# Kernel optimization log

Hardware: AMD Instinct MI355X
Metric: run time of the kernel (lower is better)

The kernel has to match this reference:

```python
import jax, jax.numpy as jnp
import numpy as np

N = 100000   # nodes
E = 1600000  # edges
B = 256      # graphs in batch
IN_DIM = 128
OUT_DIM = 64


def setup_inputs() -> dict:
    key = jax.random.key(0)
    ks = jax.random.split(key, 8)
    x = jax.random.normal(ks[0], (N, IN_DIM), dtype=jnp.float32)
    edge_index = jax.random.randint(ks[1], (2, E), 0, N)
    edge_weight = jax.random.uniform(ks[2], (E,), dtype=jnp.float32)
    batch = jnp.sort(jax.random.randint(ks[3], (N,), 0, B))
    # learned params (GCNConv: x @ W + b with glorot-ish scale)
    W1 = jax.random.normal(ks[4], (IN_DIM, OUT_DIM), dtype=jnp.float32) * 0.05
    b1 = jnp.zeros((OUT_DIM,), dtype=jnp.float32)
    W2 = jax.random.normal(ks[5], (OUT_DIM, OUT_DIM), dtype=jnp.float32) * 0.05
    b2 = jnp.zeros((OUT_DIM,), dtype=jnp.float32)
    return {"x": x, "edge_index": edge_index, "edge_weight": edge_weight,
            "batch": batch, "W1": W1, "b1": b1, "W2": W2, "b2": b2}


def _gcn_conv(x, W, b, src, dst, w, n):
    # PyG GCNConv (normalize=True, add_self_loops already applied by caller):
    # out[dst] += D^-1/2[src] * w * D^-1/2[dst] * (x @ W)[src]
    xw = x @ W
    deg = jax.ops.segment_sum(w, dst, num_segments=n)
    dinv = jnp.where(deg > 0, jax.lax.rsqrt(deg), 0.0)
    norm = dinv[src] * w * dinv[dst]
    out = jax.ops.segment_sum(norm[:, None] * xw[src], dst, num_segments=n)
    return out + b


def reference(x, edge_index, edge_weight, batch, W1, b1, W2, b2):
    n = x.shape[0]
    loop = jnp.arange(n)
    # add self loops with weight 1 (GCNConv default fill_value=1.0)
    src = jnp.concatenate([edge_index[0], loop])
    dst = jnp.concatenate([edge_index[1], loop])
    w = jnp.concatenate([edge_weight, jnp.ones((n,), x.dtype)])

    h = _gcn_conv(x, W1, b1, src, dst, w, n)
    h = _gcn_conv(h, W2, b2, src, dst, w, n)

    # deterministic pairwise clustering (stand-in for randomized graclus matching)
    n_clusters = n // 2
    cluster = loop // 2
    # max_pool_x: per-cluster feature max, cluster batch id = min over members
    xp = jax.ops.segment_max(h, cluster, num_segments=n_clusters)
    bp = jax.ops.segment_min(batch, cluster, num_segments=n_clusters)
    # original loop: x[ind[0]:ind[1]].mean(0) over contiguous batch indices is a
    # single row => output per graph = first pooled node of that graph
    first = jax.ops.segment_min(jnp.arange(n_clusters), bp, num_segments=B)
    return xp[first]
```

## Files before the change

### kernel.cpp

```cpp
#include <hip/hip_runtime.h>
#include <climits>


#define NF_CAP 40960
#define CHUNK 8192
#define STRIDE 128
#define BK_BITS 8
#define NBMAX 512
#define MAXW 3200

__global__ void k_init(unsigned int* mark1w, unsigned char* mark2,
                       int* first, int* cnt, int* gcur, float* WW, float* bW,
                       const float* __restrict__ W1, const float* __restrict__ W2,
                       const float* __restrict__ b1, int n, int nb) {
  int i = blockIdx.x * blockDim.x + threadIdx.x;
  if (i < n) mark2[i] = 0;
  if (i < MAXW) mark1w[i] = 0;
  if (i < nb) first[i] = INT_MAX;
  if (i < 4) cnt[i] = 0;
  if (i < NBMAX) gcur[i] = 0;
  int t = threadIdx.x;
  int lane = t & 63, wv = t >> 6;
  if (blockIdx.x < 2) {
    int k0 = blockIdx.x * 64 + wv * 16;
#pragma unroll 1
    for (int k = k0; k < k0 + 16; ++k) {
      float acc = 0.f;
#pragma unroll 8
      for (int m = 0; m < 64; ++m)
        acc += W1[k * 64 + m] * W2[m * 64 + lane];
      WW[k * 64 + lane] = acc;
    }
  } else if (blockIdx.x == 2 && wv == 0) {
    float acc = 0.f;
#pragma unroll 8
    for (int m = 0; m < 64; ++m)
      acc += b1[m] * W2[m * 64 + lane];
    bW[lane] = acc;
  }
}

__global__ void k_firstsel(const int* __restrict__ batch, int* first,
                           unsigned int* mark1w, unsigned char* mark2,
                           int nc, int n) {
  int c = blockIdx.x * blockDim.x + threadIdx.x;
  if (c == 0) {
    mark2[n - 2] = 1; mark2[n - 1] = 1;
    atomicOr(&mark1w[(n - 2) >> 5], 1u << ((n - 2) & 31));
    atomicOr(&mark1w[(n - 1) >> 5], 1u << ((n - 1) & 31));
  }
  if (c >= nc) return;
  int b = batch[2 * c];
  if (c == 0 || batch[2 * c - 2] != b) {
    first[b] = c;
    int n0 = 2 * c;
    mark2[n0] = 1; mark2[n0 + 1] = 1;
    atomicOr(&mark1w[n0 >> 5], 3u << (n0 & 31));
  }
}

__global__ __launch_bounds__(1024) void k_bkt(const int* __restrict__ src,
    const int* __restrict__ dst, const float* __restrict__ w,
    const unsigned int* __restrict__ mark1w, unsigned char* mark2,
    int* gcur, uint2* bktbuf, int cap, int e) {
  __shared__ int scnt[NBMAX], sgb[NBMAX];
  int t = threadIdx.x;
  if (t < NBMAX) scnt[t] = 0;
  __syncthreads();
  int i0 = blockIdx.x * CHUNK;
  int rd[8], rs[8];
  float rw[8];
#pragma unroll
  for (int k = 0; k < 8; ++k) {
    int i = i0 + t + k * 1024;
    if (i < e) {
      int d = dst[i];
      int s = src[i];
      rd[k] = d; rs[k] = s; rw[k] = w[i];
      atomicAdd(&scnt[d >> BK_BITS], 1);
      if ((mark1w[d >> 5] >> (d & 31)) & 1u) mark2[s] = 1;
    } else {
      rd[k] = -1;
    }
  }
  __syncthreads();
  if (t < NBMAX) {
    int c = scnt[t];
    sgb[t] = c ? atomicAdd(&gcur[t], c) : 0;
    scnt[t] = 0;
  }
  __syncthreads();
#pragma unroll
  for (int k = 0; k < 8; ++k) {
    if (rd[k] >= 0) {
      int b = rd[k] >> BK_BITS;
      int pos = sgb[b] + atomicAdd(&scnt[b], 1);
      if (pos < cap)
        bktbuf[(size_t)b * cap + pos] =
            make_uint2(((unsigned int)rs[k] << BK_BITS) | (unsigned int)(rd[k] & 255),
                       __float_as_uint(rw[k]));
    }
  }
}

__global__ __launch_bounds__(256) void k_degscat(const int* __restrict__ gcur,
    const uint2* __restrict__ bktbuf, int cap, const unsigned char* __restrict__ mark2,
    int* cntF, int* fidx, int* list,
    float* dinv, int* counts2, int* fcols, float* fvals, int n) {
  __shared__ float acc[256];
  __shared__ int sfidx[256];
  __shared__ int lcur[256];
  __shared__ int sd[256];
  __shared__ int base_s;
  int t = threadIdx.x, b = blockIdx.x;
  int gbase = b << BK_BITS;
  int i = gbase + t;
  acc[t] = 0.f;
  int flag = (i < n && mark2[i]) ? 1 : 0;
  sd[t] = flag;
  __syncthreads();
  for (int off = 1; off < 256; off <<= 1) {
    int a = (t >= off) ? sd[t - off] : 0;
    __syncthreads();
    sd[t] += a;
    __syncthreads();
  }
  int incl = sd[t];
  if (t == 255) base_s = atomicAdd(cntF, incl);
  __syncthreads();
  int f0 = -1;
  if (flag) {
    int g = base_s + incl - 1;
    if (g < NF_CAP) { f0 = g; fidx[i] = g; list[g] = i; }
  }
  sfidx[t] = f0;
  lcur[t] = (f0 >= 0) ? f0 * STRIDE : 0;
  __syncthreads();
  int m = min(gcur[b], cap);
  const uint2* base = bktbuf + (size_t)b * cap;
  for (int j = t; j < m; j += 256) {
    uint2 u = base[j];
    int dl = (int)(u.x & 255u);
    float wv = __uint_as_float(u.y);
    atomicAdd(&acc[dl], wv);
    int f = sfidx[dl];
    if (f >= 0) {
      int pos = atomicAdd(&lcur[dl], 1);
      if (pos < (f + 1) * STRIDE) {
        fcols[pos] = (int)(u.x >> BK_BITS);
        fvals[pos] = wv;
      }
    }
  }
  __syncthreads();
  if (i < n) {
    dinv[i] = rsqrtf(1.0f + acc[t]);
    int f = sfidx[t];
    if (f >= 0) counts2[f] = min(lcur[t] - f * STRIDE, STRIDE);
  }
}

__global__ __launch_bounds__(256) void k_agg(const float* __restrict__ x,
    const int* __restrict__ list, const int* __restrict__ cntF,
    const int* __restrict__ counts2, const int* __restrict__ fcols,
    const float* __restrict__ fvals, const float* __restrict__ dinv,
    float* __restrict__ aggx) {
  int lane = threadIdx.x & 63;
  int half = lane >> 5, sub = lane & 31;
  int wid = (blockIdx.x * blockDim.x + threadIdx.x) >> 6;
  int nw = (gridDim.x * blockDim.x) >> 6;
  int m = min(*cntF, NF_CAP);
  const float4* x4 = (const float4*)x;
  float4* a4 = (float4*)aggx;
  for (int li = wid; li < m; li += nw) {
    int i = list[li];
    float dv = dinv[i];
    float4 xi = x4[(size_t)i * 32 + sub];
    float ax = 0.f, ay = 0.f, az = 0.f, aw = 0.f;
    int p = li * STRIDE;
    int end = p + counts2[li];
    while (p + 16 <= end) {
      int c[8]; float v[8]; float4 g[8];
#pragma unroll
      for (int j = 0; j < 8; ++j) {
        c[j] = fcols[p + 2 * j + half];
        v[j] = fvals[p + 2 * j + half];
      }
#pragma unroll
      for (int j = 0; j < 8; ++j) g[j] = x4[(size_t)c[j] * 32 + sub];
#pragma unroll
      for (int j = 0; j < 8; ++j) v[j] *= dinv[c[j]];
#pragma unroll
      for (int j = 0; j < 8; ++j) {
        ax += v[j] * g[j].x; ay += v[j] * g[j].y;
        az += v[j] * g[j].z; aw += v[j] * g[j].w;
      }
      p += 16;
    }
    while (p + 4 <= end) {
      int c0 = fcols[p + half], c1 = fcols[p + 2 + half];
      float v0 = fvals[p + half], v1 = fvals[p + 2 + half];
      float4 g0 = x4[(size_t)c0 * 32 + sub];
      float4 g1 = x4[(size_t)c1 * 32 + sub];
      v0 *= dinv[c0]; v1 *= dinv[c1];
      ax += v0 * g0.x + v1 * g1.x; ay += v0 * g0.y + v1 * g1.y;
      az += v0 * g0.z + v1 * g1.z; aw += v0 * g0.w + v1 * g1.w;
      p += 4;
    }
    while (p + 2 <= end) {
      int c = fcols[p + half];
      float v = fvals[p + half] * dinv[c];
      float4 g = x4[(size_t)c * 32 + sub];
      ax += v * g.x; ay += v * g.y; az += v * g.z; aw += v * g.w;
      p += 2;
    }
    if (p < end && half == 0) {
      int c = fcols[p];
      float v = fvals[p] * dinv[c];
      float4 g = x4[(size_t)c * 32 + sub];
      ax += v * g.x; ay += v * g.y; az += v * g.z; aw += v * g.w;
    }
    ax += __shfl(ax, lane ^ 32);
    ay += __shfl(ay, lane ^ 32);
    az += __shfl(az, lane ^ 32);
    aw += __shfl(aw, lane ^ 32);
    if (half == 0) {
      float4 r;
      r.x = dv * (ax + dv * xi.x);
      r.y = dv * (ay + dv * xi.y);
      r.z = dv * (az + dv * xi.z);
      r.w = dv * (aw + dv * xi.w);
      a4[(size_t)li * 32 + sub] = r;
    }
  }
}

__global__ __launch_bounds__(128) void k_h2out(const float* __restrict__ aggx,
    const int* __restrict__ first, const int* __restrict__ fidx,
    const int* __restrict__ counts2, const int* __restrict__ fcols,
    const float* __restrict__ fvals, const float* __restrict__ dinv,
    const float* __restrict__ WW, const float* __restrict__ bW,
    const float* __restrict__ b2, float* __restrict__ out, int nb, int nc) {
  __shared__ float Wl[128 * 64];
  __shared__ float sag[2][128];
  __shared__ float hh[2][64];
  int t = threadIdx.x;
  for (int p = t; p < 128 * 16; p += 128)
    ((float4*)Wl)[p] = ((const float4*)WW)[p];
  __syncthreads();
  int lane = t & 63, wv = t >> 6;
  int half = lane >> 5, sub = lane & 31;
  int b = blockIdx.x;
  if (b >= nb) return;
  int fc = min(first[b], nc - 1);
  int node = 2 * fc + wv;
  int f = fidx[node];
  float dv = dinv[node];
  const float4* a4 = (const float4*)aggx;
  float ax = 0.f, ay = 0.f, az = 0.f, aw = 0.f, sv = 0.f;
  int p = f * STRIDE;
  int end = p + counts2[f];
  while (p + 8 <= end) {
    int c[4]; float v[4]; int g[4]; float4 r[4];
#pragma unroll
    for (int j = 0; j < 4; ++j) {
      c[j] = fcols[p + 2 * j + half];
      v[j] = fvals[p + 2 * j + half];
    }
#pragma unroll
    for (int j = 0; j < 4; ++j) g[j] = fidx[c[j]];
#pragma unroll
    for (int j = 0; j < 4; ++j) v[j] *= dinv[c[j]];
#pragma unroll
    for (int j = 0; j < 4; ++j) r[j] = a4[(size_t)g[j] * 32 + sub];
#pragma unroll
    for (int j = 0; j < 4; ++j) {
      ax += v[j] * r[j].x; ay += v[j] * r[j].y;
      az += v[j] * r[j].z; aw += v[j] * r[j].w;
      sv += v[j];
    }
    p += 8;
  }
  while (p + 2 <= end) {
    int c = fcols[p + half];
    float v = fvals[p + half] * dinv[c];
    int g = fidx[c];
    float4 r = a4[(size_t)g * 32 + sub];
    ax += v * r.x; ay += v * r.y; az += v * r.z; aw += v * r.w;
    sv += v;
    p += 2;
  }
  if (p < end && half == 0) {
    int c = fcols[p];
    float v = fvals[p] * dinv[c];
    int g = fidx[c];
    float4 r = a4[(size_t)g * 32 + sub];
    ax += v * r.x; ay += v * r.y; az += v * r.z; aw += v * r.w;
    sv += v;
  }
  ax += __shfl(ax, lane ^ 32);
  ay += __shfl(ay, lane ^ 32);
  az += __shfl(az, lane ^ 32);
  aw += __shfl(aw, lane ^ 32);
  sv += __shfl(sv, lane ^ 32);
  float4 rs = a4[(size_t)f * 32 + sub];
  if (half == 0) {
    sag[wv][4 * sub + 0] = dv * (ax + dv * rs.x);
    sag[wv][4 * sub + 1] = dv * (ay + dv * rs.y);
    sag[wv][4 * sub + 2] = dv * (az + dv * rs.z);
    sag[wv][4 * sub + 3] = dv * (aw + dv * rs.w);
  }
  float sfin = dv * (sv + dv);
  __syncthreads();
  float o = b2[lane] + sfin * bW[lane];
#pragma unroll 8
  for (int k = 0; k < 128; ++k)
    o += sag[wv][k] * Wl[k * 64 + lane];
  hh[wv][lane] = o;
  __syncthreads();
  if (wv == 0)
    out[(size_t)b * 64 + lane] = fmaxf(hh[0][lane], hh[1][lane]);
}

extern "C" void kernel_launch(void* const* d_in, const int* in_sizes, int n_in,
                              void* d_out, int out_size, void* d_ws, size_t ws_size,
                              hipStream_t stream) {
  const float* x     = (const float*)d_in[0];
  const int*   ei    = (const int*)d_in[1];
  const float* ew    = (const float*)d_in[2];
  const int*   batch = (const int*)d_in[3];
  const float* W1    = (const float*)d_in[4];
  const float* b1    = (const float*)d_in[5];
  const float* W2    = (const float*)d_in[6];
  const float* b2    = (const float*)d_in[7];

  const int E  = in_sizes[2];
  const int N  = in_sizes[3];
  const int B  = out_size / 64;
  const int NC = N / 2;
  const int* srcI = ei;
  const int* dstI = ei + E;

  const int NBKT = (N + 255) >> BK_BITS;
  const int CAP  = ((E + NBKT - 1) / NBKT) * 2;

  char* p = (char*)d_ws;
  auto alloc = [&](size_t bytes) -> char* {
    char* r = p;
    p += (bytes + 255) & ~size_t(255);
    return r;
  };
  float* dinv    = (float*)alloc((size_t)N * 4);
  unsigned int* mark1w = (unsigned int*)alloc((size_t)MAXW * 4);
  unsigned char* mark2 = (unsigned char*)alloc(N);
  int*   fidx    = (int*)alloc((size_t)N * 4);
  int*   list    = (int*)alloc((size_t)NF_CAP * 4);
  int*   counts2 = (int*)alloc((size_t)NF_CAP * 4);
  int*   first   = (int*)alloc((size_t)B * 4);
  int*   cnt     = (int*)alloc(256);
  int*   gcur    = (int*)alloc(NBMAX * 4);
  float* WW      = (float*)alloc(128 * 64 * 4);
  float* bW      = (float*)alloc(64 * 4);
  uint2* bktbuf  = (uint2*)alloc((size_t)NBKT * CAP * 8);
  int*   fcols   = (int*)alloc((size_t)NF_CAP * STRIDE * 4);
  float* fvals   = (float*)alloc((size_t)NF_CAP * STRIDE * 4);
  float* aggx    = (float*)alloc((size_t)NF_CAP * 128 * 4);

  int gN = (N + 255) / 256;
  int gB = (E + CHUNK - 1) / CHUNK;
  int* cntF = cnt;

  k_init<<<gN, 256, 0, stream>>>(mark1w, mark2, first, cnt, gcur, WW, bW,
                                 W1, W2, b1, N, B);
  k_firstsel<<<(NC + 255) / 256, 256, 0, stream>>>(batch, first, mark1w, mark2, NC, N);
  k_bkt<<<gB, 1024, 0, stream>>>(srcI, dstI, ew, mark1w, mark2, gcur, bktbuf, CAP, E);
  k_degscat<<<NBKT, 256, 0, stream>>>(gcur, bktbuf, CAP, mark2, cntF, fidx, list,
                                      dinv, counts2, fcols, fvals, N);
  k_agg<<<2048, 256, 0, stream>>>(x, list, cntF, counts2, fcols, fvals, dinv, aggx);
  k_h2out<<<B, 128, 0, stream>>>(aggx, first, fidx, counts2, fcols, fvals, dinv,
                                 WW, bW, b2, (float*)d_out, B, NC);
}
```

Before: 99.50 us.

## Replace global-atomic bucket cursors with per-block slab slots and prefix scan

Edge bucketing no longer reserves space in each destination bucket with global atomicAdd on a shared cursor. Each source block now writes into its own fixed 64-entry slot per bucket and records a per-block count. The degree/scatter kernel prefix-scans those counts and finds each entry's slot by binary search. This removes global atomic contention and lets k_init clear mark2 with int-wide stores, at the cost of a scan, a binary search per element, and silently dropping edges when a block holds more than 64 for one bucket.

New measurement: 107.4 us. 7.9% more time.

```diff
diff --git a/kernel.cpp b/kernel.cpp
--- a/kernel.cpp
+++ b/kernel.cpp
@@ -8,17 +8,17 @@
 #define BK_BITS 8
 #define NBMAX 512
 #define MAXW 3200
-
-__global__ void k_init(unsigned int* mark1w, unsigned char* mark2,
-                       int* first, int* cnt, int* gcur, float* WW, float* bW,
+#define SLOT 64
+
+__global__ void k_init(unsigned int* mark1w, int* mark2i,
+                       int* first, int* cnt, float* WW, float* bW,
                        const float* __restrict__ W1, const float* __restrict__ W2,
-                       const float* __restrict__ b1, int n, int nb) {
+                       const float* __restrict__ b1, int n4, int nb) {
   int i = blockIdx.x * blockDim.x + threadIdx.x;
-  if (i < n) mark2[i] = 0;
+  if (i < n4) mark2i[i] = 0;
   if (i < MAXW) mark1w[i] = 0;
   if (i < nb) first[i] = INT_MAX;
   if (i < 4) cnt[i] = 0;
-  if (i < NBMAX) gcur[i] = 0;
   int t = threadIdx.x;
   int lane = t & 63, wv = t >> 6;
   if (blockIdx.x < 2) {
@@ -62,12 +62,13 @@
 __global__ __launch_bounds__(1024) void k_bkt(const int* __restrict__ src,
     const int* __restrict__ dst, const float* __restrict__ w,
     const unsigned int* __restrict__ mark1w, unsigned char* mark2,
-    int* gcur, uint2* bktbuf, int cap, int e) {
-  __shared__ int scnt[NBMAX], sgb[NBMAX];
+    int* cnt, uint2* slab, int e, int nbkt, int nblk) {
+  __shared__ int scnt[NBMAX];
   int t = threadIdx.x;
   if (t < NBMAX) scnt[t] = 0;
   __syncthreads();
-  int i0 = blockIdx.x * CHUNK;
+  int g = blockIdx.x;
+  int i0 = g * CHUNK;
   int rd[8], rs[8];
   float rw[8];
 #pragma unroll
@@ -84,9 +85,8 @@
     }
   }
   __syncthreads();
-  if (t < NBMAX) {
-    int c = scnt[t];
-    sgb[t] = c ? atomicAdd(&gcur[t], c) : 0;
+  if (t < nbkt) {
+    cnt[g * nbkt + t] = min(scnt[t], SLOT);
     scnt[t] = 0;
   }
   __syncthreads();
@@ -94,23 +94,25 @@
   for (int k = 0; k < 8; ++k) {
     if (rd[k] >= 0) {
       int b = rd[k] >> BK_BITS;
-      int pos = sgb[b] + atomicAdd(&scnt[b], 1);
-      if (pos < cap)
-        bktbuf[(size_t)b * cap + pos] =
+      int pos = atomicAdd(&scnt[b], 1);
+      if (pos < SLOT)
+        slab[((size_t)b * nblk + g) * SLOT + pos] =
             make_uint2(((unsigned int)rs[k] << BK_BITS) | (unsigned int)(rd[k] & 255),
                        __float_as_uint(rw[k]));
     }
   }
 }
 
-__global__ __launch_bounds__(256) void k_degscat(const int* __restrict__ gcur,
-    const uint2* __restrict__ bktbuf, int cap, const unsigned char* __restrict__ mark2,
+__global__ __launch_bounds__(256) void k_degscat(const int* __restrict__ cnt,
+    const uint2* __restrict__ slab, int nblk, int nbkt,
+    const unsigned char* __restrict__ mark2,
     int* cntF, int* fidx, int* list,
     float* dinv, int* counts2, int* fcols, float* fvals, int n) {
   __shared__ float acc[256];
   __shared__ int sfidx[256];
   __shared__ int lcur[256];
   __shared__ int sd[256];
+  __shared__ int pref[257];
   __shared__ int base_s;
   int t = threadIdx.x, b = blockIdx.x;
   int gbase = b << BK_BITS;
@@ -130,25 +132,44 @@
   __syncthreads();
   int f0 = -1;
   if (flag) {
-    int g = base_s + incl - 1;
-    if (g < NF_CAP) { f0 = g; fidx[i] = g; list[g] = i; }
+    int gidx = base_s + incl - 1;
+    if (gidx < NF_CAP) { f0 = gidx; fidx[i] = gidx; list[gidx] = i; }
   }
   sfidx[t] = f0;
   lcur[t] = (f0 >= 0) ? f0 * STRIDE : 0;
-  __syncthreads();
-  int m = min(gcur[b], cap);
-  const uint2* base = bktbuf + (size_t)b * cap;
-  for (int j = t; j < m; j += 256) {
-    uint2 u = base[j];
-    int dl = (int)(u.x & 255u);
-    float wv = __uint_as_float(u.y);
-    atomicAdd(&acc[dl], wv);
-    int f = sfidx[dl];
-    if (f >= 0) {
-      int pos = atomicAdd(&lcur[dl], 1);
-      if (pos < (f + 1) * STRIDE) {
-        fcols[pos] = (int)(u.x >> BK_BITS);
-        fvals[pos] = wv;
+  int v = (t < nblk) ? cnt[t * nbkt + b] : 0;
+  sd[t] = v;
+  __syncthreads();
+  for (int off = 1; off < 256; off <<= 1) {
+    int a = (t >= off) ? sd[t - off] : 0;
+    __syncthreads();
+    sd[t] += a;
+    __syncthreads();
+  }
+  pref[t + 1] = sd[t];
+  if (t == 0) pref[0] = 0;
+  __syncthreads();
+  int m = pref[nblk];
+  const uint2* sb = slab + (size_t)b * nblk * SLOT;
+  for (int j0 = 0; j0 < m; j0 += 256) {
+    int j = j0 + t;
+    if (j < m) {
+      int lo = 0, hi = nblk;
+      while (hi - lo > 1) {
+        int mid = (lo + hi) >> 1;
+        if (pref[mid] <= j) lo = mid; else hi = mid;
+      }
+      uint2 u = sb[(size_t)lo * SLOT + (j - pref[lo])];
+      int dl = (int)(u.x & 255u);
+      float wv = __uint_as_float(u.y);
+      atomicAdd(&acc[dl], wv);
+      int f = sfidx[dl];
+      if (f >= 0) {
+        int pos = atomicAdd(&lcur[dl], 1);
+        if (pos < (f + 1) * STRIDE) {
+          fcols[pos] = (int)(u.x >> BK_BITS);
+          fvals[pos] = wv;
+        }
       }
     }
   }
@@ -342,7 +363,7 @@
   const int* dstI = ei + E;
 
   const int NBKT = (N + 255) >> BK_BITS;
-  const int CAP  = ((E + NBKT - 1) / NBKT) * 2;
+  const int NBLK = (E + CHUNK - 1) / CHUNK;
 
   char* p = (char*)d_ws;
   auto alloc = [&](size_t bytes) -> char* {
@@ -352,30 +373,31 @@
   };
   float* dinv    = (float*)alloc((size_t)N * 4);
   unsigned int* mark1w = (unsigned int*)alloc((size_t)MAXW * 4);
-  unsigned char* mark2 = (unsigned char*)alloc(N);
+  unsigned char* mark2 = (unsigned char*)alloc((size_t)(N + 4));
   int*   fidx    = (int*)alloc((size_t)N * 4);
   int*   list    = (int*)alloc((size_t)NF_CAP * 4);
   int*   counts2 = (int*)alloc((size_t)NF_CAP * 4);
   int*   first   = (int*)alloc((size_t)B * 4);
   int*   cnt     = (int*)alloc(256);
-  int*   gcur    = (int*)alloc(NBMAX * 4);
+  int*   bcnt    = (int*)alloc((size_t)NBLK * NBKT * 4);
   float* WW      = (float*)alloc(128 * 64 * 4);
   float* bW      = (float*)alloc(64 * 4);
-  uint2* bktbuf  = (uint2*)alloc((size_t)NBKT * CAP * 8);
+  uint2* slab    = (uint2*)alloc((size_t)NBKT * NBLK * SLOT * 8);
   int*   fcols   = (int*)alloc((size_t)NF_CAP * STRIDE * 4);
   float* fvals   = (float*)alloc((size_t)NF_CAP * STRIDE * 4);
   float* aggx    = (float*)alloc((size_t)NF_CAP * 128 * 4);
 
-  int gN = (N + 255) / 256;
-  int gB = (E + CHUNK - 1) / CHUNK;
+  const int N4 = (N + 3) / 4;
+  int gI = (N4 + 255) / 256;
   int* cntF = cnt;
 
-  k_init<<<gN, 256, 0, stream>>>(mark1w, mark2, first, cnt, gcur, WW, bW,
-                                 W1, W2, b1, N, B);
+  k_init<<<gI, 256, 0, stream>>>(mark1w, (int*)mark2, first, cnt, WW, bW,
+                                 W1, W2, b1, N4, B);
   k_firstsel<<<(NC + 255) / 256, 256, 0, stream>>>(batch, first, mark1w, mark2, NC, N);
-  k_bkt<<<gB, 1024, 0, stream>>>(srcI, dstI, ew, mark1w, mark2, gcur, bktbuf, CAP, E);
-  k_degscat<<<NBKT, 256, 0, stream>>>(gcur, bktbuf, CAP, mark2, cntF, fidx, list,
-                                      dinv, counts2, fcols, fvals, N);
+  k_bkt<<<NBLK, 1024, 0, stream>>>(srcI, dstI, ew, mark1w, mark2, bcnt, slab,
+                                   E, NBKT, NBLK);
+  k_degscat<<<NBKT, 256, 0, stream>>>(bcnt, slab, NBLK, NBKT, mark2, cntF, fidx,
+                                      list, dinv, counts2, fcols, fvals, N);
   k_agg<<<2048, 256, 0, stream>>>(x, list, cntF, counts2, fcols, fvals, dinv, aggx);
   k_h2out<<<B, 128, 0, stream>>>(aggx, first, fidx, counts2, fcols, fvals, dinv,
                                  WW, bW, b2, (float*)d_out, B, NC);
```
